# Performance work log

Measured on AMD Instinct MI355X. Metric: run time of the kernel, lower is better.

Reference implementation:

```python
import jax, jax.numpy as jnp
import numpy as np
from jax import lax

H = 8
C_HID = 32
LIDAR_DIM = 20
LIMITS = np.array([[1.0, 1.0, 3.1415927]], dtype=np.float32)


def _lidar_encoder(scans, w1, b1, w2, b2, wl, bl):
    # scans: [N, 20] -> Conv1d(1->16,k5,p2), ReLU, MaxPool(2), Conv1d(16->32,k3,p1), ReLU, global avg, Linear(32->5), ReLU
    x = scans[:, None, :]
    x = lax.conv_general_dilated(x, w1, (1,), [(2, 2)], dimension_numbers=('NCH', 'OIH', 'NCH')) + b1[None, :, None]
    x = jax.nn.relu(x)
    x = lax.reduce_window(x, -jnp.inf, lax.max, (1, 1, 2), (1, 1, 2), 'VALID')  # [N,16,10]
    x = lax.conv_general_dilated(x, w2, (1,), [(1, 1)], dimension_numbers=('NCH', 'OIH', 'NCH')) + b2[None, :, None]
    x = jax.nn.relu(x)
    x = jnp.mean(x, axis=2)  # AdaptiveAvgPool1d(1)+Flatten -> [N,32]
    return jax.nn.relu(x @ wl.T + bl)


def _gat_conv(x, src, dst, edge_attr, W, a_src, a_dst, We, a_e, bias, N):
    # PyG GATConv, heads=H, concat=True, edge_dim=1, leaky_relu slope 0.2, softmax over incoming edges (dst)
    xw = (x @ W).reshape(N, H, C_HID)
    als = jnp.sum(xw * a_src[None], -1)  # [N,H]
    ald = jnp.sum(xw * a_dst[None], -1)  # [N,H]
    ef = (edge_attr @ We).reshape(-1, H, C_HID)
    ale = jnp.sum(ef * a_e[None], -1)    # [E,H]
    alpha = jax.nn.leaky_relu(als[src] + ald[dst] + ale, 0.2)
    amax = jax.ops.segment_max(alpha, dst, num_segments=N)
    ex = jnp.exp(alpha - amax[dst])
    denom = jax.ops.segment_sum(ex, dst, num_segments=N)
    coef = ex / (denom[dst] + 1e-16)
    out = jax.ops.segment_sum(coef[:, :, None] * xw[src], dst, num_segments=N)
    return out.reshape(N, H * C_HID) + bias


def setup_inputs() -> dict:
    key = jax.random.key(0)
    ks = jax.random.split(key, 40)
    B, NPG, A = 1024, 16, 8
    N = B * NPG
    nodes = np.arange(NPG)
    s, d = np.meshgrid(nodes, nodes, indexing='ij')
    m = s != d
    s, d = s[m], d[m]  # fully-connected directed, no self loops (240 edges/graph)
    off = (np.arange(B) * NPG)[:, None]
    src = (off + s[None, :]).reshape(-1)
    dst = (off + d[None, :]).reshape(-1)
    E = src.shape[0]
    hid = C_HID
    def nrm(k, shape, sc=0.1):
        return jax.random.normal(k, shape, dtype=jnp.float32) * sc
    return {
        'x': jax.random.normal(ks[0], (N, 29), dtype=jnp.float32),
        'edge_index': jnp.asarray(np.stack([src, dst]).astype(np.int32)),
        'edge_attr': jax.random.uniform(ks[1], (E, 1), dtype=jnp.float32),
        'batch': jnp.asarray(np.repeat(np.arange(B), NPG).astype(np.int32)),
        'num_graphs': B,
        'num_agents': A,
        'lc_w1': nrm(ks[2], (16, 1, 5)), 'lc_b1': nrm(ks[3], (16,)),
        'lc_w2': nrm(ks[4], (32, 16, 3)), 'lc_b2': nrm(ks[5], (32,)),
        'lc_wl': nrm(ks[6], (5, 32)), 'lc_bl': nrm(ks[7], (5,)),
        'ld_w1': nrm(ks[8], (hid, 5)), 'ld_b1': nrm(ks[9], (hid,)),
        'ld_w2': nrm(ks[10], (LIDAR_DIM, hid)), 'ld_b2': nrm(ks[11], (LIDAR_DIM,)),
        'g1_W': nrm(ks[12], (6, H * hid)), 'g1_asrc': nrm(ks[13], (H, hid)), 'g1_adst': nrm(ks[14], (H, hid)), 'g1_We': nrm(ks[15], (1, H * hid)), 'g1_ae': nrm(ks[16], (H, hid)), 'g1_b': nrm(ks[17], (H * hid,)),
        'g2_W': nrm(ks[18], (H * hid, H * hid)), 'g2_asrc': nrm(ks[19], (H, hid)), 'g2_adst': nrm(ks[20], (H, hid)), 'g2_We': nrm(ks[21], (1, H * hid)), 'g2_ae': nrm(ks[22], (H, hid)), 'g2_b': nrm(ks[23], (H * hid,)),
        'g3_W': nrm(ks[24], (H * hid, H * hid)), 'g3_asrc': nrm(ks[25], (H, hid)), 'g3_adst': nrm(ks[26], (H, hid)), 'g3_We': nrm(ks[27], (1, H * hid)), 'g3_ae': nrm(ks[28], (H, hid)), 'g3_b': nrm(ks[29], (H * hid,)),
        'fc1_W': nrm(ks[30], (4 * hid, 16 * hid + 3)), 'fc1_b': nrm(ks[31], (4 * hid,)),
        'fc2_W': nrm(ks[32], (6, 4 * hid)), 'fc2_b': nrm(ks[33], (6,)),
    }


def reference(x, edge_index, edge_attr, batch, num_graphs, num_agents,
              lc_w1, lc_b1, lc_w2, lc_b2, lc_wl, lc_bl,
              ld_w1, ld_b1, ld_w2, ld_b2,
              g1_W, g1_asrc, g1_adst, g1_We, g1_ae, g1_b,
              g2_W, g2_asrc, g2_adst, g2_We, g2_ae, g2_b,
              g3_W, g3_asrc, g3_adst, g3_We, g3_ae, g3_b,
              fc1_W, fc1_b, fc2_W, fc2_b):
    N = x.shape[0]
    scans = x[:, :LIDAR_DIM]
    orig = x[:, LIDAR_DIM:LIDAR_DIM + 6]
    last_act = x[:, LIDAR_DIM + 6:]
    z = _lidar_encoder(scans, lc_w1, lc_b1, lc_w2, lc_b2, lc_wl, lc_bl)
    recon = jax.nn.relu(z @ ld_w1.T + ld_b1) @ ld_w2.T + ld_b2
    src, dst = edge_index[0], edge_index[1]
    # conv1: add_self_loops=False
    h = jax.nn.relu(_gat_conv(orig, src, dst, edge_attr, g1_W, g1_asrc, g1_adst, g1_We, g1_ae, g1_b, N))
    # conv2/conv3: add_self_loops=True with fill_value='mean' for edge_attr
    loop = jnp.arange(N, dtype=src.dtype)
    src2 = jnp.concatenate([src, loop])
    dst2 = jnp.concatenate([dst, loop])
    ea2 = jnp.concatenate([edge_attr, jnp.broadcast_to(jnp.mean(edge_attr, axis=0, keepdims=True), (N, 1))], axis=0)
    h = jax.nn.relu(_gat_conv(h, src2, dst2, ea2, g2_W, g2_asrc, g2_adst, g2_We, g2_ae, g2_b, N))
    h = jax.nn.relu(_gat_conv(h, src2, dst2, ea2, g3_W, g3_asrc, g3_adst, g3_We, g3_ae, g3_b, N))
    counts = jax.ops.segment_sum(jnp.ones((N,), jnp.float32), batch, num_segments=num_graphs)
    gemb = jax.ops.segment_sum(h, batch, num_segments=num_graphs) / counts[:, None]
    starts = jnp.searchsorted(batch, jnp.arange(num_graphs, dtype=batch.dtype))
    idx = (starts[:, None] + jnp.arange(num_agents)).reshape(-1)
    aemb = h[idx]
    la = last_act[idx]
    grep = jnp.repeat(gemb, num_agents, axis=0)
    comb = jnp.concatenate([aemb, grep, la], axis=1)
    hidn = jax.nn.relu(comb @ fc1_W.T + fc1_b)
    p = hidn @ fc2_W.T + fc2_b
    mean = jnp.tanh(p[:, :3]) * jnp.asarray(LIMITS)
    std = 0.01 + jax.nn.sigmoid(p[:, 3:]) * (0.3 - 0.01) + 1e-05
    return (mean.reshape(num_graphs, num_agents, -1), std.reshape(num_graphs, num_agents, -1), scans, recon)
```

## Files before the change

### kernel.cpp

```cpp
#include <hip/hip_runtime.h>
#include <math.h>

#define NODES   16384
#define NGRAPH  1024
#define EDGES   245760
#define EPG     240
#define FDIM    256

#define OUT_MEAN  0
#define OUT_STD   24576
#define OUT_SCANS 49152
#define OUT_RECON 376832

typedef __attribute__((ext_vector_type(4))) short bf16x4;
typedef __attribute__((ext_vector_type(8))) short bf16x8;
typedef __attribute__((ext_vector_type(4))) float f32x4;

static __device__ __forceinline__ float lrelu02(float v){ return v > 0.f ? v : 0.2f*v; }

static __device__ __forceinline__ unsigned short f2bf(float f){
    unsigned u = __float_as_uint(f);
    u = (u + 0x7FFFu + ((u >> 16) & 1u)) >> 16;
    return (unsigned short)u;
}
static __device__ __forceinline__ float bf2f(unsigned short h){
    return __uint_as_float(((unsigned)h) << 16);
}

__global__ __launch_bounds__(256) void prep_kernel(
    const float* __restrict__ x,  const float* __restrict__ ea,
    const float* __restrict__ W2, const float* __restrict__ as2, const float* __restrict__ ad2,
    const float* __restrict__ W3, const float* __restrict__ as3, const float* __restrict__ ad3,
    const float* __restrict__ W1, const float* __restrict__ as1, const float* __restrict__ ad1,
    const float* __restrict__ F1,
    const float* __restrict__ w1, const float* __restrict__ b1,
    const float* __restrict__ w2, const float* __restrict__ b2,
    const float* __restrict__ wl, const float* __restrict__ bl,
    const float* __restrict__ dw1, const float* __restrict__ db1,
    const float* __restrict__ dw2, const float* __restrict__ db2,
    unsigned short* __restrict__ T2, unsigned short* __restrict__ T3,
    unsigned short* __restrict__ T1, float* __restrict__ W1E,
    float* __restrict__ partial, float* __restrict__ out)
{
    __shared__ float red[256];
    __shared__ float sc[8][25];
    __shared__ float pooled[8][160];
    __shared__ float hid_lds[8][32];

    const int b = blockIdx.x;
    const int tid = threadIdx.x;

    if (b < 68) {
        const float* W   = (b < 34) ? W2 : W3;
        const float* as_ = (b < 34) ? as2 : as3;
        const float* ad_ = (b < 34) ? ad2 : ad3;
        unsigned short* T = (b < 34) ? T2 : T3;
        const int slot = ((b < 34) ? b : b - 34) * 256 + tid;
        const int nt = slot >> 9;
        const int rem = slot & 511;
        const int kk = rem >> 6;
        const int lane = rem & 63;
        const int ar = lane & 15, kgg = lane >> 4;
        const int col = nt * 16 + ar;
        unsigned short vals[8];
#pragma unroll
        for (int j = 0; j < 8; ++j) {
            const int k = kk * 32 + kgg * 4 + (j & 3) + ((j >> 2) << 4);
            float v;
            if (col < 256) v = W[k * 256 + col];
            else {
                const int j2 = col - 256, h = j2 & 7;
                const float* av = (j2 < 8) ? as_ : ad_;
                float s = 0.f;
                for (int c = 0; c < 32; ++c) s += W[k * 256 + h * 32 + c] * av[h * 32 + c];
                v = s;
            }
            vals[j] = f2bf(v);
        }
        *(bf16x8*)(T + (size_t)slot * 8) = *(const bf16x8*)vals;
        return;
    }
    if (b < 100) {
        const int slot = (b - 68) * 256 + tid;
        const int nt = slot >> 10;
        const int rem = slot & 1023;
        const int kk = rem >> 6;
        const int lane = rem & 63;
        const int o = nt * 16 + (lane & 15);
        const int kgg = lane >> 4;
        unsigned short vals[8];
#pragma unroll
        for (int j = 0; j < 8; ++j) {
            const int k = kk * 32 + kgg * 4 + (j & 3) + ((j >> 2) << 4);
            vals[j] = f2bf(F1[o * 515 + k]);
        }
        *(bf16x8*)(T1 + (size_t)slot * 8) = *(const bf16x8*)vals;
        return;
    }
    if (b == 100) {
        for (int c = tid; c < 272; c += 256) {
            for (int k = 0; k < 6; ++k) {
                float v;
                if (c < 256) v = W1[k * 256 + c];
                else {
                    const int j = c - 256, h = j & 7;
                    const float* av = (j < 8) ? as1 : ad1;
                    float s = 0.f;
                    for (int cc = 0; cc < 32; ++cc) s += W1[k * 256 + h * 32 + cc] * av[h * 32 + cc];
                    v = s;
                }
                W1E[k * 272 + c] = v;
            }
        }
        return;
    }
    if (b < 357) {
        const int base = (b - 101) * 960;
        float s = 0.f;
        for (int i = tid; i < 960; i += 256) s += ea[base + i];
        red[tid] = s; __syncthreads();
        for (int off = 128; off > 0; off >>= 1) {
            if (tid < off) red[tid] += red[tid + off];
            __syncthreads();
        }
        if (tid == 0) partial[b - 101] = red[0];
        return;
    }

    const int lane = tid & 31;
    const int nl   = tid >> 5;
    const int n    = (b - 357) * 8 + nl;

    if (lane < 20) {
        const float v = x[n * 29 + lane];
        sc[nl][lane + 2] = v;
        out[OUT_SCANS + n * 20 + lane] = v;
    } else if (lane < 25) {
        const int pads[5] = {0, 1, 22, 23, 24};
        sc[nl][pads[lane - 20]] = 0.f;
    }
    __syncthreads();

    {
        const int ic = lane & 15;
        const int hi = lane >> 4;
        float w1r[5];
#pragma unroll
        for (int k = 0; k < 5; ++k) w1r[k] = w1[ic * 5 + k];
        const float b1r = b1[ic];
#pragma unroll
        for (int q = 0; q < 5; ++q) {
            const int u  = 2 * q + hi;
            const int p0 = 2 * u;
            float a = b1r, bb = b1r;
#pragma unroll
            for (int k = 0; k < 5; ++k) {
                a  += sc[nl][p0 + k] * w1r[k];
                bb += sc[nl][p0 + 1 + k] * w1r[k];
            }
            pooled[nl][u * 16 + ic] = fmaxf(fmaxf(a, bb), 0.f);
        }
    }
    __syncthreads();

    float macc = 0.f;
    {
        float wreg[48];
#pragma unroll
        for (int i = 0; i < 12; ++i) {
            const float4 v4 = *(const float4*)&w2[lane * 48 + i * 4];
            wreg[i * 4 + 0] = v4.x; wreg[i * 4 + 1] = v4.y;
            wreg[i * 4 + 2] = v4.z; wreg[i * 4 + 3] = v4.w;
        }
        const float b2r = b2[lane];
        float pc[3][16];
#pragma unroll
        for (int i = 0; i < 4; ++i) {
            const float4 v0 = *(const float4*)&pooled[nl][0 * 16 + i * 4];
            const float4 v1 = *(const float4*)&pooled[nl][1 * 16 + i * 4];
            pc[0][i * 4 + 0] = v0.x; pc[0][i * 4 + 1] = v0.y; pc[0][i * 4 + 2] = v0.z; pc[0][i * 4 + 3] = v0.w;
            pc[1][i * 4 + 0] = v1.x; pc[1][i * 4 + 1] = v1.y; pc[1][i * 4 + 2] = v1.z; pc[1][i * 4 + 3] = v1.w;
            pc[2][i * 4 + 0] = 0.f;  pc[2][i * 4 + 1] = 0.f;  pc[2][i * 4 + 2] = 0.f;  pc[2][i * 4 + 3] = 0.f;
        }
#pragma unroll
        for (int t = 0; t < 10; ++t) {
            const int prev = (t + 2) % 3, cur = t % 3, nxt = (t + 1) % 3;
            if (t >= 1) {
                if (t + 1 <= 9) {
#pragma unroll
                    for (int i = 0; i < 4; ++i) {
                        const float4 v4 = *(const float4*)&pooled[nl][(t + 1) * 16 + i * 4];
                        pc[nxt][i * 4 + 0] = v4.x; pc[nxt][i * 4 + 1] = v4.y;
                        pc[nxt][i * 4 + 2] = v4.z; pc[nxt][i * 4 + 3] = v4.w;
                    }
                } else {
#pragma unroll
                    for (int ic = 0; ic < 16; ++ic) pc[nxt][ic] = 0.f;
                }
            }
            float v = b2r;
#pragma unroll
            for (int ic = 0; ic < 16; ++ic) {
                v += pc[prev][ic] * wreg[ic * 3 + 0]
                   + pc[cur][ic]  * wreg[ic * 3 + 1]
                   + pc[nxt][ic]  * wreg[ic * 3 + 2];
            }
            macc += fmaxf(v, 0.f);
        }
    }

    const float feat = macc * 0.1f;
    float z[5];
#pragma unroll
    for (int j = 0; j < 5; ++j) {
        float p = feat * wl[j * 32 + lane];
        p += __shfl_xor(p, 1);
        p += __shfl_xor(p, 2);
        p += __shfl_xor(p, 4);
        p += __shfl_xor(p, 8);
        p += __shfl_xor(p, 16);
        z[j] = fmaxf(bl[j] + p, 0.f);
    }
    float hv = db1[lane];
#pragma unroll
    for (int j = 0; j < 5; ++j) hv += z[j] * dw1[lane * 5 + j];
    hid_lds[nl][lane] = fmaxf(hv, 0.f);
    __syncthreads();

    if (lane < 20) {
        float acc = db2[lane];
#pragma unroll
        for (int k = 0; k < 32; ++k) acc += hid_lds[nl][k] * dw2[lane * 32 + k];
        out[OUT_RECON + n * 20 + lane] = acc;
    }
}

__global__ __launch_bounds__(512) void graph_kernel(
    const float* __restrict__ x,   const float* __restrict__ ea,
    const float* __restrict__ partial,
    const float* __restrict__ W1E,
    const float* __restrict__ g1_We, const float* __restrict__ g1_ae,
    const float* __restrict__ g1_b,
    const unsigned short* __restrict__ WTEf2,
    const float* __restrict__ g2_We, const float* __restrict__ g2_ae,
    const float* __restrict__ g2_b,
    const unsigned short* __restrict__ WTEf3,
    const float* __restrict__ g3_We, const float* __restrict__ g3_ae,
    const float* __restrict__ g3_b,
    const unsigned short* __restrict__ FT1f,
    const float* __restrict__ fc1W, const float* __restrict__ fc1b,
    const float* __restrict__ fc2W, const float* __restrict__ fc2b,
    float* __restrict__ out)
{
    __shared__ char hsb[2][8192] __attribute__((aligned(16)));
    __shared__ float salsald[2][16][16];
    __shared__ unsigned short coefb[2][8][16][20] __attribute__((aligned(8)));
    __shared__ float sS[8];
    __shared__ float hs6[2][16][6];
    __shared__ float lash[2][8][3];
    __shared__ float hidn[16][132];
    __shared__ unsigned short gembb[2][256] __attribute__((aligned(8)));
    __shared__ float ealds[480];

    const int tid = threadIdx.x;
    const int g0 = blockIdx.x * 2;
    const int lane = tid & 63, w = tid >> 6;
    const int arow = lane & 15, kg = lane >> 4;

    float eamean;
    {
        float pv = partial[lane] + partial[lane + 64] + partial[lane + 128] + partial[lane + 192];
        pv += __shfl_xor(pv, 1);
        pv += __shfl_xor(pv, 2);
        pv += __shfl_xor(pv, 4);
        pv += __shfl_xor(pv, 8);
        pv += __shfl_xor(pv, 16);
        pv += __shfl_xor(pv, 32);
        eamean = pv * (1.f / (float)EDGES);
    }

    if (tid < 192) {
        const int gg = tid / 96, t = tid % 96;
        hs6[gg][t / 6][t % 6] = x[((g0 + gg) * 16 + t / 6) * 29 + 20 + t % 6];
    } else if (tid < 240) {
        const int t = tid - 192, gg = t / 24, r = t % 24;
        lash[gg][r / 3][r % 3] = x[((g0 + gg) * 16 + r / 3) * 29 + 26 + r % 3];
    } else if (tid >= 248 && tid < 256) {
        const int h = tid - 248;
        float s = 0.f;
        for (int c = 0; c < 32; ++c) s += g1_We[h * 32 + c] * g1_ae[h * 32 + c];
        sS[h] = s;
    } else if (tid >= 256) {
        const int t = tid - 256;
        ealds[t] = ea[g0 * EPG + t];
        if (t < 224) ealds[t + 256] = ea[g0 * EPG + t + 256];
    }
    __syncthreads();

    float colA[16];
    {
        const int gg = tid >> 8, ht = tid & 255;
#pragma unroll
        for (int i = 0; i < 16; ++i) colA[i] = 0.f;
#pragma unroll
        for (int k = 0; k < 6; ++k) {
            const float wa = W1E[k * 272 + ht];
#pragma unroll
            for (int i = 0; i < 16; ++i) colA[i] += hs6[gg][i][k] * wa;
        }
        if (ht < 16) {
            float colC[16];
#pragma unroll
            for (int i = 0; i < 16; ++i) colC[i] = 0.f;
#pragma unroll
            for (int k = 0; k < 6; ++k) {
                const float wc = W1E[k * 272 + 256 + ht];
#pragma unroll
                for (int i = 0; i < 16; ++i) colC[i] += hs6[gg][i][k] * wc;
            }
#pragma unroll
            for (int i = 0; i < 16; ++i) salsald[gg][i][ht] = colC[i];
        }
    }
    __syncthreads();

    if (tid < 256) {
        const int gg = tid >> 7, row = tid & 127;
        const int d = row >> 3, h = row & 7;
        const float S = sS[h];
        const float aldv = salsald[gg][d][8 + h];
        float alf[16];
        float m = -1e30f;
#pragma unroll
        for (int s = 0; s < 16; ++s) {
            float a;
            if (s == d) a = -1e30f;
            else {
                const int el = s * 15 + d - (d > s ? 1 : 0);
                a = lrelu02(salsald[gg][s][h] + aldv + ealds[gg * EPG + el] * S);
            }
            alf[s] = a;
            m = fmaxf(m, a);
        }
        float sum = 0.f;
#pragma unroll
        for (int s = 0; s < 16; ++s) { alf[s] = expf(alf[s] - m); sum += alf[s]; }
        const float r = 1.f / (sum + 1e-16f);
#pragma unroll
        for (int s = 0; s < 16; ++s) coefb[gg][h][d][s] = f2bf(alf[s] * r);
    }
    __syncthreads();

    {
        const int gg = tid >> 8, c = tid & 255;
        const int h = c >> 5;
        const float b = g1_b[c];
#pragma unroll
        for (int d = 0; d < 16; ++d) {
            float v = b;
#pragma unroll
            for (int s4 = 0; s4 < 4; ++s4) {
                const bf16x4 cv = *(const bf16x4*)((const char*)&coefb[gg][0][0][0] + h * 640 + d * 40 + s4 * 8);
                v += bf2f((unsigned short)cv[0]) * colA[s4 * 4 + 0]
                   + bf2f((unsigned short)cv[1]) * colA[s4 * 4 + 1]
                   + bf2f((unsigned short)cv[2]) * colA[s4 * 4 + 2]
                   + bf2f((unsigned short)cv[3]) * colA[s4 * 4 + 3];
            }
            *(unsigned short*)(hsb[gg] + ((d * 512 + c * 2) ^ ((d & 7) << 4))) = f2bf(fmaxf(v, 0.f));
        }
    }
    __syncthreads();

#pragma unroll 1
    for (int ly = 0; ly < 2; ++ly) {
        const unsigned short* WT = ly ? WTEf3 : WTEf2;
        const float* We_ = ly ? g3_We : g2_We;
        const float* ae_ = ly ? g3_ae : g2_ae;
        const float* bi_ = ly ? g3_b  : g2_b;

        if (tid < 8) {
            float s = 0.f;
            for (int c = 0; c < 32; ++c) s += We_[tid * 32 + c] * ae_[tid * 32 + c];
            sS[tid] = s;
        }

        f32x4 acc[3][2];
#pragma unroll
        for (int t = 0; t < 3; ++t) { acc[t][0] = (f32x4){0,0,0,0}; acc[t][1] = (f32x4){0,0,0,0}; }
        {
            const int aswz = (arow & 7) << 4;
            for (int kk = 0; kk < 8; ++kk) {
                bf16x8 afr[2];
#pragma unroll
                for (int gg = 0; gg < 2; ++gg) {
                    const int ab = arow * 512 + kk * 64 + kg * 8;
                    const bf16x4 alo = *(const bf16x4*)(hsb[gg] + (ab ^ aswz));
                    const bf16x4 ahi = *(const bf16x4*)(hsb[gg] + ((ab + 32) ^ aswz));
                    afr[gg] = (bf16x8){alo[0], alo[1], alo[2], alo[3],
                                       ahi[0], ahi[1], ahi[2], ahi[3]};
                }
#pragma unroll
                for (int t = 0; t < 2; ++t) {
                    const int nt = t * 8 + w;
                    const bf16x8 bfr = *(const bf16x8*)(WT + (size_t)((nt * 8 + kk) * 64 + lane) * 8);
                    acc[t][0] = __builtin_amdgcn_mfma_f32_16x16x32_bf16(afr[0], bfr, acc[t][0], 0, 0, 0);
                    acc[t][1] = __builtin_amdgcn_mfma_f32_16x16x32_bf16(afr[1], bfr, acc[t][1], 0, 0, 0);
                }
                if (w == 0) {
                    const bf16x8 bfr = *(const bf16x8*)(WT + (size_t)((16 * 8 + kk) * 64 + lane) * 8);
                    acc[2][0] = __builtin_amdgcn_mfma_f32_16x16x32_bf16(afr[0], bfr, acc[2][0], 0, 0, 0);
                    acc[2][1] = __builtin_amdgcn_mfma_f32_16x16x32_bf16(afr[1], bfr, acc[2][1], 0, 0, 0);
                }
            }
        }
        if (w == 0) {
#pragma unroll
            for (int gg = 0; gg < 2; ++gg)
#pragma unroll
                for (int r = 0; r < 4; ++r) salsald[gg][kg * 4 + r][arow] = acc[2][gg][r];
        }
        __syncthreads();

        if (tid < 256) {
            const int gg = tid >> 7, row = tid & 127;
            const int d = row >> 3, h = row & 7;
            const float S = sS[h];
            const float aldv = salsald[gg][d][8 + h];
            float alf[16];
            float m = -1e30f;
#pragma unroll
            for (int s = 0; s < 16; ++s) {
                float a;
                if (s == d) a = lrelu02(salsald[gg][s][h] + aldv + eamean * S);
                else {
                    const int el = s * 15 + d - (d > s ? 1 : 0);
                    a = lrelu02(salsald[gg][s][h] + aldv + ealds[gg * EPG + el] * S);
                }
                alf[s] = a;
                m = fmaxf(m, a);
            }
            float sum = 0.f;
#pragma unroll
            for (int s = 0; s < 16; ++s) { alf[s] = expf(alf[s] - m); sum += alf[s]; }
            const float r = 1.f / (sum + 1e-16f);
#pragma unroll
            for (int s = 0; s < 16; ++s) coefb[gg][h][d][s] = f2bf(alf[s] * r);
        }
        __syncthreads();

        {
#pragma unroll
            for (int t = 0; t < 2; ++t) {
                const int nt = t * 8 + w;
                const int h = nt >> 1;
                const int c2 = nt * 16 + arow;
#pragma unroll
                for (int gg = 0; gg < 2; ++gg) {
                    const bf16x4 alo = *(const bf16x4*)((const char*)&coefb[gg][0][0][0] + h * 640 + arow * 40 + kg * 8);
                    const bf16x8 afrag = (bf16x8){alo[0], alo[1], alo[2], alo[3], 0, 0, 0, 0};
                    const bf16x8 bfr = (bf16x8){
                        (short)f2bf(acc[t][gg][0]), (short)f2bf(acc[t][gg][1]),
                        (short)f2bf(acc[t][gg][2]), (short)f2bf(acc[t][gg][3]),
                        0, 0, 0, 0};
                    f32x4 hacc = __builtin_amdgcn_mfma_f32_16x16x32_bf16(
                                     afrag, bfr, (f32x4){0.f, 0.f, 0.f, 0.f}, 0, 0, 0);
                    const float b = bi_[c2];
                    float p = 0.f;
#pragma unroll
                    for (int r = 0; r < 4; ++r) {
                        const float hv = fmaxf(hacc[r] + b, 0.f);
                        p += hv;
                        const int d = kg * 4 + r;
                        *(unsigned short*)(hsb[gg] + ((d * 512 + c2 * 2) ^ ((d & 7) << 4))) = f2bf(hv);
                    }
                    if (ly == 1) {
                        p += __shfl_xor(p, 16);
                        p += __shfl_xor(p, 32);
                        if (kg == 0) gembb[gg][c2] = f2bf(p * (1.f / 16.f));
                    }
                }
            }
        }
        __syncthreads();
    }

    {
        f32x4 acc2 = (f32x4){0,0,0,0};
        const int agg = arow >> 3, alr = arow & 7;
        const int aswz = (alr & 7) << 4;
        for (int kk = 0; kk < 16; ++kk) {
            bf16x4 alo, ahi;
            if (kk < 8) {
                const int ab = alr * 512 + kk * 64 + kg * 8;
                alo = *(const bf16x4*)(hsb[agg] + (ab ^ aswz));
                ahi = *(const bf16x4*)(hsb[agg] + ((ab + 32) ^ aswz));
            } else {
                const char* gp = (const char*)&gembb[agg][0] + (kk - 8) * 64 + kg * 8;
                alo = *(const bf16x4*)(gp);
                ahi = *(const bf16x4*)(gp + 32);
            }
            const bf16x8 afrag = (bf16x8){alo[0], alo[1], alo[2], alo[3],
                                          ahi[0], ahi[1], ahi[2], ahi[3]};
            const bf16x8 bfr = *(const bf16x8*)(FT1f + (size_t)((w * 16 + kk) * 64 + lane) * 8);
            acc2 = __builtin_amdgcn_mfma_f32_16x16x32_bf16(afrag, bfr, acc2, 0, 0, 0);
        }
        {
            const int o = w * 16 + arow;
            const float wl0 = fc1W[o * 515 + 512];
            const float wl1 = fc1W[o * 515 + 513];
            const float wl2 = fc1W[o * 515 + 514];
            const float b   = fc1b[o];
#pragma unroll
            for (int r = 0; r < 4; ++r) {
                const int row = kg * 4 + r;
                const int gg = row >> 3, ag = row & 7;
                float v = acc2[r] + b
                        + lash[gg][ag][0] * wl0 + lash[gg][ag][1] * wl1 + lash[gg][ag][2] * wl2;
                hidn[row][o] = fmaxf(v, 0.f);
            }
        }
    }
    __syncthreads();

    if (tid < 96) {
        const int a = tid / 6, j = tid % 6;
        const float* wr = &fc2W[j * 128];
        float acc = fc2b[j];
#pragma unroll
        for (int k = 0; k < 128; ++k) acc += wr[k] * hidn[a][k];
        const int gg = a >> 3, ag = a & 7;
        const int base = ((g0 + gg) * 8 + ag) * 3;
        if (j < 3) {
            const float lim = (j == 2) ? 3.1415927f : 1.0f;
            out[OUT_MEAN + base + j] = tanhf(acc) * lim;
        } else {
            const float sg = 1.f / (1.f + expf(-acc));
            out[OUT_STD + base + (j - 3)] = 0.01f + sg * (0.3f - 0.01f) + 1e-5f;
        }
    }
}

extern "C" void kernel_launch(void* const* d_in, const int* in_sizes, int n_in,
                              void* d_out, int out_size, void* d_ws, size_t ws_size,
                              hipStream_t stream)
{
    const float* x     = (const float*)d_in[0];
    const float* ea    = (const float*)d_in[2];
    const float* lc_w1 = (const float*)d_in[6];
    const float* lc_b1 = (const float*)d_in[7];
    const float* lc_w2 = (const float*)d_in[8];
    const float* lc_b2 = (const float*)d_in[9];
    const float* lc_wl = (const float*)d_in[10];
    const float* lc_bl = (const float*)d_in[11];
    const float* ld_w1 = (const float*)d_in[12];
    const float* ld_b1 = (const float*)d_in[13];
    const float* ld_w2 = (const float*)d_in[14];
    const float* ld_b2 = (const float*)d_in[15];
    const float* g1_W  = (const float*)d_in[16];
    const float* g1_as = (const float*)d_in[17];
    const float* g1_ad = (const float*)d_in[18];
    const float* g1_We = (const float*)d_in[19];
    const float* g1_ae = (const float*)d_in[20];
    const float* g1_b  = (const float*)d_in[21];
    const float* g2_W  = (const float*)d_in[22];
    const float* g2_as = (const float*)d_in[23];
    const float* g2_ad = (const float*)d_in[24];
    const float* g2_We = (const float*)d_in[25];
    const float* g2_ae = (const float*)d_in[26];
    const float* g2_b  = (const float*)d_in[27];
    const float* g3_W  = (const float*)d_in[28];
    const float* g3_as = (const float*)d_in[29];
    const float* g3_ad = (const float*)d_in[30];
    const float* g3_We = (const float*)d_in[31];
    const float* g3_ae = (const float*)d_in[32];
    const float* g3_b  = (const float*)d_in[33];
    const float* fc1_W = (const float*)d_in[34];
    const float* fc1_b = (const float*)d_in[35];
    const float* fc2_W = (const float*)d_in[36];
    const float* fc2_b = (const float*)d_in[37];

    float* out = (float*)d_out;
    unsigned short* WTEf2 = (unsigned short*)d_ws;
    unsigned short* WTEf3 = WTEf2 + 8704 * 8;
    unsigned short* FT1f  = WTEf3 + 8704 * 8;
    float* W1E    = (float*)(FT1f + 8192 * 8);
    float* partial = W1E + 6 * 272;

    prep_kernel<<<2405, 256, 0, stream>>>(x, ea,
                                          g2_W, g2_as, g2_ad,
                                          g3_W, g3_as, g3_ad,
                                          g1_W, g1_as, g1_ad,
                                          fc1_W,
                                          lc_w1, lc_b1, lc_w2, lc_b2, lc_wl, lc_bl,
                                          ld_w1, ld_b1, ld_w2, ld_b2,
                                          WTEf2, WTEf3, FT1f, W1E, partial, out);

    graph_kernel<<<512, 512, 0, stream>>>(x, ea, partial,
                                          W1E, g1_We, g1_ae, g1_b,
                                          WTEf2, g2_We, g2_ae, g2_b,
                                          WTEf3, g3_We, g3_ae, g3_b,
                                          FT1f, fc1_W, fc1_b, fc2_W, fc2_b, out);
}
```

Baseline: 73.51 us.

## Move lidar encoder/decoder blocks from prep kernel into graph kernel

The per-node lidar conv encoder and reconstruction decoder move out of the prep kernel and into extra blocks (index >= 512) of the graph kernel. These blocks process 16 nodes each and reuse the graph kernel's shared buffer. The prep kernel shrinks to the weight-packing and edge-attribute reduction blocks, so the critical path before the graph kernel gets shorter and the lidar work can overlap with the graph blocks. The cost is that the graph kernel's grid grows to 1536 blocks of 512 threads, with the larger LDS and register footprint of the graph path possibly limiting occupancy for the lidar blocks.

```diff
diff --git a/kernel.cpp b/kernel.cpp
--- a/kernel.cpp
+++ b/kernel.cpp
@@ -28,25 +28,16 @@
 }
 
 __global__ __launch_bounds__(256) void prep_kernel(
-    const float* __restrict__ x,  const float* __restrict__ ea,
+    const float* __restrict__ ea,
     const float* __restrict__ W2, const float* __restrict__ as2, const float* __restrict__ ad2,
     const float* __restrict__ W3, const float* __restrict__ as3, const float* __restrict__ ad3,
     const float* __restrict__ W1, const float* __restrict__ as1, const float* __restrict__ ad1,
     const float* __restrict__ F1,
-    const float* __restrict__ w1, const float* __restrict__ b1,
-    const float* __restrict__ w2, const float* __restrict__ b2,
-    const float* __restrict__ wl, const float* __restrict__ bl,
-    const float* __restrict__ dw1, const float* __restrict__ db1,
-    const float* __restrict__ dw2, const float* __restrict__ db2,
     unsigned short* __restrict__ T2, unsigned short* __restrict__ T3,
     unsigned short* __restrict__ T1, float* __restrict__ W1E,
-    float* __restrict__ partial, float* __restrict__ out)
+    float* __restrict__ partial)
 {
     __shared__ float red[256];
-    __shared__ float sc[8][25];
-    __shared__ float pooled[8][160];
-    __shared__ float hid_lds[8][32];
-
     const int b = blockIdx.x;
     const int tid = threadIdx.x;
 
@@ -114,7 +105,7 @@
         }
         return;
     }
-    if (b < 357) {
+    {
         const int base = (b - 101) * 960;
         float s = 0.f;
         for (int i = tid; i < 960; i += 256) s += ea[base + i];
@@ -124,114 +115,6 @@
             __syncthreads();
         }
         if (tid == 0) partial[b - 101] = red[0];
-        return;
-    }
-
-    const int lane = tid & 31;
-    const int nl   = tid >> 5;
-    const int n    = (b - 357) * 8 + nl;
-
-    if (lane < 20) {
-        const float v = x[n * 29 + lane];
-        sc[nl][lane + 2] = v;
-        out[OUT_SCANS + n * 20 + lane] = v;
-    } else if (lane < 25) {
-        const int pads[5] = {0, 1, 22, 23, 24};
-        sc[nl][pads[lane - 20]] = 0.f;
-    }
-    __syncthreads();
-
-    {
-        const int ic = lane & 15;
-        const int hi = lane >> 4;
-        float w1r[5];
-#pragma unroll
-        for (int k = 0; k < 5; ++k) w1r[k] = w1[ic * 5 + k];
-        const float b1r = b1[ic];
-#pragma unroll
-        for (int q = 0; q < 5; ++q) {
-            const int u  = 2 * q + hi;
-            const int p0 = 2 * u;
-            float a = b1r, bb = b1r;
-#pragma unroll
-            for (int k = 0; k < 5; ++k) {
-                a  += sc[nl][p0 + k] * w1r[k];
-                bb += sc[nl][p0 + 1 + k] * w1r[k];
-            }
-            pooled[nl][u * 16 + ic] = fmaxf(fmaxf(a, bb), 0.f);
-        }
-    }
-    __syncthreads();
-
-    float macc = 0.f;
-    {
-        float wreg[48];
-#pragma unroll
-        for (int i = 0; i < 12; ++i) {
-            const float4 v4 = *(const float4*)&w2[lane * 48 + i * 4];
-            wreg[i * 4 + 0] = v4.x; wreg[i * 4 + 1] = v4.y;
-            wreg[i * 4 + 2] = v4.z; wreg[i * 4 + 3] = v4.w;
-        }
-        const float b2r = b2[lane];
-        float pc[3][16];
-#pragma unroll
-        for (int i = 0; i < 4; ++i) {
-            const float4 v0 = *(const float4*)&pooled[nl][0 * 16 + i * 4];
-            const float4 v1 = *(const float4*)&pooled[nl][1 * 16 + i * 4];
-            pc[0][i * 4 + 0] = v0.x; pc[0][i * 4 + 1] = v0.y; pc[0][i * 4 + 2] = v0.z; pc[0][i * 4 + 3] = v0.w;
-            pc[1][i * 4 + 0] = v1.x; pc[1][i * 4 + 1] = v1.y; pc[1][i * 4 + 2] = v1.z; pc[1][i * 4 + 3] = v1.w;
-            pc[2][i * 4 + 0] = 0.f;  pc[2][i * 4 + 1] = 0.f;  pc[2][i * 4 + 2] = 0.f;  pc[2][i * 4 + 3] = 0.f;
-        }
-#pragma unroll
-        for (int t = 0; t < 10; ++t) {
-            const int prev = (t + 2) % 3, cur = t % 3, nxt = (t + 1) % 3;
-            if (t >= 1) {
-                if (t + 1 <= 9) {
-#pragma unroll
-                    for (int i = 0; i < 4; ++i) {
-                        const float4 v4 = *(const float4*)&pooled[nl][(t + 1) * 16 + i * 4];
-                        pc[nxt][i * 4 + 0] = v4.x; pc[nxt][i * 4 + 1] = v4.y;
-                        pc[nxt][i * 4 + 2] = v4.z; pc[nxt][i * 4 + 3] = v4.w;
-                    }
-                } else {
-#pragma unroll
-                    for (int ic = 0; ic < 16; ++ic) pc[nxt][ic] = 0.f;
-                }
-            }
-            float v = b2r;
-#pragma unroll
-            for (int ic = 0; ic < 16; ++ic) {
-                v += pc[prev][ic] * wreg[ic * 3 + 0]
-                   + pc[cur][ic]  * wreg[ic * 3 + 1]
-                   + pc[nxt][ic]  * wreg[ic * 3 + 2];
-            }
-            macc += fmaxf(v, 0.f);
-        }
-    }
-
-    const float feat = macc * 0.1f;
-    float z[5];
-#pragma unroll
-    for (int j = 0; j < 5; ++j) {
-        float p = feat * wl[j * 32 + lane];
-        p += __shfl_xor(p, 1);
-        p += __shfl_xor(p, 2);
-        p += __shfl_xor(p, 4);
-        p += __shfl_xor(p, 8);
-        p += __shfl_xor(p, 16);
-        z[j] = fmaxf(bl[j] + p, 0.f);
-    }
-    float hv = db1[lane];
-#pragma unroll
-    for (int j = 0; j < 5; ++j) hv += z[j] * dw1[lane * 5 + j];
-    hid_lds[nl][lane] = fmaxf(hv, 0.f);
-    __syncthreads();
-
-    if (lane < 20) {
-        float acc = db2[lane];
-#pragma unroll
-        for (int k = 0; k < 32; ++k) acc += hid_lds[nl][k] * dw2[lane * 32 + k];
-        out[OUT_RECON + n * 20 + lane] = acc;
     }
 }
 
@@ -250,6 +133,11 @@
     const unsigned short* __restrict__ FT1f,
     const float* __restrict__ fc1W, const float* __restrict__ fc1b,
     const float* __restrict__ fc2W, const float* __restrict__ fc2b,
+    const float* __restrict__ w1, const float* __restrict__ b1,
+    const float* __restrict__ w2, const float* __restrict__ b2,
+    const float* __restrict__ wl, const float* __restrict__ bl,
+    const float* __restrict__ dw1, const float* __restrict__ db1,
+    const float* __restrict__ dw2, const float* __restrict__ db2,
     float* __restrict__ out)
 {
     __shared__ char hsb[2][8192] __attribute__((aligned(16)));
@@ -263,6 +151,121 @@
     __shared__ float ealds[480];
 
     const int tid = threadIdx.x;
+
+    if (blockIdx.x >= 512) {
+        float* scb = (float*)&hsb[0][0];
+        float* plb = scb + 16 * 25;
+        float* hdb = plb + 16 * 160;
+
+        const int lane = tid & 31;
+        const int nl   = tid >> 5;
+        const int n    = (blockIdx.x - 512) * 16 + nl;
+
+        if (lane < 20) {
+            const float v = x[n * 29 + lane];
+            scb[nl * 25 + lane + 2] = v;
+            out[OUT_SCANS + n * 20 + lane] = v;
+        } else if (lane < 25) {
+            const int pads[5] = {0, 1, 22, 23, 24};
+            scb[nl * 25 + pads[lane - 20]] = 0.f;
+        }
+        __syncthreads();
+
+        {
+            const int ic = lane & 15;
+            const int hi = lane >> 4;
+            float w1r[5];
+#pragma unroll
+            for (int k = 0; k < 5; ++k) w1r[k] = w1[ic * 5 + k];
+            const float b1r = b1[ic];
+#pragma unroll
+            for (int q = 0; q < 5; ++q) {
+                const int u  = 2 * q + hi;
+                const int p0 = 2 * u;
+                float a = b1r, bb = b1r;
+#pragma unroll
+                for (int k = 0; k < 5; ++k) {
+                    a  += scb[nl * 25 + p0 + k] * w1r[k];
+                    bb += scb[nl * 25 + p0 + 1 + k] * w1r[k];
+                }
+                plb[nl * 160 + u * 16 + ic] = fmaxf(fmaxf(a, bb), 0.f);
+            }
+        }
+        __syncthreads();
+
+        float macc = 0.f;
+        {
+            float wreg[48];
+#pragma unroll
+            for (int i = 0; i < 12; ++i) {
+                const float4 v4 = *(const float4*)&w2[lane * 48 + i * 4];
+                wreg[i * 4 + 0] = v4.x; wreg[i * 4 + 1] = v4.y;
+                wreg[i * 4 + 2] = v4.z; wreg[i * 4 + 3] = v4.w;
+            }
+            const float b2r = b2[lane];
+            float pc[3][16];
+#pragma unroll
+            for (int i = 0; i < 4; ++i) {
+                const float4 v0 = *(const float4*)&plb[nl * 160 + 0 * 16 + i * 4];
+                const float4 v1 = *(const float4*)&plb[nl * 160 + 1 * 16 + i * 4];
+                pc[0][i * 4 + 0] = v0.x; pc[0][i * 4 + 1] = v0.y; pc[0][i * 4 + 2] = v0.z; pc[0][i * 4 + 3] = v0.w;
+                pc[1][i * 4 + 0] = v1.x; pc[1][i * 4 + 1] = v1.y; pc[1][i * 4 + 2] = v1.z; pc[1][i * 4 + 3] = v1.w;
+                pc[2][i * 4 + 0] = 0.f;  pc[2][i * 4 + 1] = 0.f;  pc[2][i * 4 + 2] = 0.f;  pc[2][i * 4 + 3] = 0.f;
+            }
+#pragma unroll
+            for (int t = 0; t < 10; ++t) {
+                const int prev = (t + 2) % 3, cur = t % 3, nxt = (t + 1) % 3;
+                if (t >= 1) {
+                    if (t + 1 <= 9) {
+#pragma unroll
+                        for (int i = 0; i < 4; ++i) {
+                            const float4 v4 = *(const float4*)&plb[nl * 160 + (t + 1) * 16 + i * 4];
+                            pc[nxt][i * 4 + 0] = v4.x; pc[nxt][i * 4 + 1] = v4.y;
+                            pc[nxt][i * 4 + 2] = v4.z; pc[nxt][i * 4 + 3] = v4.w;
+                        }
+                    } else {
+#pragma unroll
+                        for (int ic = 0; ic < 16; ++ic) pc[nxt][ic] = 0.f;
+                    }
+                }
+                float v = b2r;
+#pragma unroll
+                for (int ic = 0; ic < 16; ++ic) {
+                    v += pc[prev][ic] * wreg[ic * 3 + 0]
+                       + pc[cur][ic]  * wreg[ic * 3 + 1]
+                       + pc[nxt][ic]  * wreg[ic * 3 + 2];
+                }
+                macc += fmaxf(v, 0.f);
+            }
+        }
+
+        const float feat = macc * 0.1f;
+        float z[5];
+#pragma unroll
+        for (int j = 0; j < 5; ++j) {
+            float p = feat * wl[j * 32 + lane];
+            p += __shfl_xor(p, 1);
+            p += __shfl_xor(p, 2);
+            p += __shfl_xor(p, 4);
+            p += __shfl_xor(p, 8);
+            p += __shfl_xor(p, 16);
+            z[j] = fmaxf(bl[j] + p, 0.f);
+        }
+        float hv = db1[lane];
+#pragma unroll
+        for (int j = 0; j < 5; ++j) hv += z[j] * dw1[lane * 5 + j];
+        hdb[nl * 32 + lane] = fmaxf(hv, 0.f);
+        __syncthreads();
+
+        if (lane < 20) {
+            float acc = db2[lane];
+#pragma unroll
+            for (int k = 0; k < 32; ++k) acc += hdb[nl * 32 + k] * dw2[lane * 32 + k];
+            out[OUT_RECON + n * 20 + lane] = acc;
+        }
+        return;
+    }
+
     const int g0 = blockIdx.x * 2;
     const int lane = tid & 63, w = tid >> 6;
     const int arow = lane & 15, kg = lane >> 4;
@@ -586,18 +589,19 @@
     float* W1E    = (float*)(FT1f + 8192 * 8);
     float* partial = W1E + 6 * 272;
 
-    prep_kernel<<<2405, 256, 0, stream>>>(x, ea,
-                                          g2_W, g2_as, g2_ad,
-                                          g3_W, g3_as, g3_ad,
-                                          g1_W, g1_as, g1_ad,
-                                          fc1_W,
-                                          lc_w1, lc_b1, lc_w2, lc_b2, lc_wl, lc_bl,
-                                          ld_w1, ld_b1, ld_w2, ld_b2,
-                                          WTEf2, WTEf3, FT1f, W1E, partial, out);
-
-    graph_kernel<<<512, 512, 0, stream>>>(x, ea, partial,
-                                          W1E, g1_We, g1_ae, g1_b,
-                                          WTEf2, g2_We, g2_ae, g2_b,
-                                          WTEf3, g3_We, g3_ae, g3_b,
-                                          FT1f, fc1_W, fc1_b, fc2_W, fc2_b, out);
+    prep_kernel<<<357, 256, 0, stream>>>(ea,
+                                         g2_W, g2_as, g2_ad,
+                                         g3_W, g3_as, g3_ad,
+                                         g1_W, g1_as, g1_ad,
+                                         fc1_W,
+                                         WTEf2, WTEf3, FT1f, W1E, partial);
+
+    graph_kernel<<<1536, 512, 0, stream>>>(x, ea, partial,
+                                           W1E, g1_We, g1_ae, g1_b,
+                                           WTEf2, g2_We, g2_ae, g2_b,
+                                           WTEf3, g3_We, g3_ae, g3_b,
+                                           FT1f, fc1_W, fc1_b, fc2_W, fc2_b,
+                                           lc_w1, lc_b1, lc_w2, lc_b2, lc_wl, lc_bl,
+                                           ld_w1, ld_b1, ld_w2, ld_b2,
+                                           out);
 }
```

Measured after the change: 88.65 us. 1.21x slower.

## Process one graph per block instead of two in graph kernel

Applied to the files above, without the earlier changes.

The graph kernel now handles a single graph per 512-thread block and launches 1024 blocks instead of 512, halving per-block shared memory and state. Each weight fragment loaded for the MFMA layers is now reused across one graph instead of two, and many threads sit idle in the scalar phases. The intent is more blocks and better occupancy, at the cost of twice the weight-fragment traffic and half-empty MFMA tiles in the final FC layer.

```diff
diff --git a/kernel.cpp b/kernel.cpp
--- a/kernel.cpp
+++ b/kernel.cpp
@@ -252,18 +252,18 @@
     const float* __restrict__ fc2W, const float* __restrict__ fc2b,
     float* __restrict__ out)
 {
-    __shared__ char hsb[2][8192] __attribute__((aligned(16)));
-    __shared__ float salsald[2][16][16];
-    __shared__ unsigned short coefb[2][8][16][20] __attribute__((aligned(8)));
+    __shared__ char hsb[8192] __attribute__((aligned(16)));
+    __shared__ float salsald[16][16];
+    __shared__ unsigned short coefb[8][16][20] __attribute__((aligned(8)));
     __shared__ float sS[8];
-    __shared__ float hs6[2][16][6];
-    __shared__ float lash[2][8][3];
-    __shared__ float hidn[16][132];
-    __shared__ unsigned short gembb[2][256] __attribute__((aligned(8)));
-    __shared__ float ealds[480];
+    __shared__ float hs6[16][6];
+    __shared__ float lash[8][3];
+    __shared__ float hidn[8][132];
+    __shared__ unsigned short gembb[256] __attribute__((aligned(8)));
+    __shared__ float ealds[240];
 
     const int tid = threadIdx.x;
-    const int g0 = blockIdx.x * 2;
+    const int g = blockIdx.x;
     const int lane = tid & 63, w = tid >> 6;
     const int arow = lane & 15, kg = lane >> 4;
 
@@ -279,56 +279,42 @@
         eamean = pv * (1.f / (float)EDGES);
     }
 
-    if (tid < 192) {
-        const int gg = tid / 96, t = tid % 96;
-        hs6[gg][t / 6][t % 6] = x[((g0 + gg) * 16 + t / 6) * 29 + 20 + t % 6];
-    } else if (tid < 240) {
-        const int t = tid - 192, gg = t / 24, r = t % 24;
-        lash[gg][r / 3][r % 3] = x[((g0 + gg) * 16 + r / 3) * 29 + 26 + r % 3];
+    if (tid < 96) {
+        hs6[tid / 6][tid % 6] = x[(g * 16 + tid / 6) * 29 + 20 + tid % 6];
+    } else if (tid < 120) {
+        const int t = tid - 96;
+        lash[t / 3][t % 3] = x[(g * 16 + t / 3) * 29 + 26 + t % 3];
     } else if (tid >= 248 && tid < 256) {
         const int h = tid - 248;
         float s = 0.f;
         for (int c = 0; c < 32; ++c) s += g1_We[h * 32 + c] * g1_ae[h * 32 + c];
         sS[h] = s;
-    } else if (tid >= 256) {
-        const int t = tid - 256;
-        ealds[t] = ea[g0 * EPG + t];
-        if (t < 224) ealds[t + 256] = ea[g0 * EPG + t + 256];
+    } else if (tid >= 256 && tid < 496) {
+        ealds[tid - 256] = ea[g * EPG + (tid - 256)];
     }
     __syncthreads();
 
     float colA[16];
-    {
-        const int gg = tid >> 8, ht = tid & 255;
+    if (tid < 272) {
 #pragma unroll
         for (int i = 0; i < 16; ++i) colA[i] = 0.f;
 #pragma unroll
         for (int k = 0; k < 6; ++k) {
-            const float wa = W1E[k * 272 + ht];
-#pragma unroll
-            for (int i = 0; i < 16; ++i) colA[i] += hs6[gg][i][k] * wa;
-        }
-        if (ht < 16) {
-            float colC[16];
-#pragma unroll
-            for (int i = 0; i < 16; ++i) colC[i] = 0.f;
-#pragma unroll
-            for (int k = 0; k < 6; ++k) {
-                const float wc = W1E[k * 272 + 256 + ht];
-#pragma unroll
-                for (int i = 0; i < 16; ++i) colC[i] += hs6[gg][i][k] * wc;
-            }
-#pragma unroll
-            for (int i = 0; i < 16; ++i) salsald[gg][i][ht] = colC[i];
-        }
-    }
-    __syncthreads();
-
-    if (tid < 256) {
-        const int gg = tid >> 7, row = tid & 127;
-        const int d = row >> 3, h = row & 7;
+            const float wa = W1E[k * 272 + tid];
+#pragma unroll
+            for (int i = 0; i < 16; ++i) colA[i] += hs6[i][k] * wa;
+        }
+        if (tid >= 256) {
+#pragma unroll
+            for (int i = 0; i < 16; ++i) salsald[i][tid - 256] = colA[i];
+        }
+    }
+    __syncthreads();
+
+    if (tid < 128) {
+        const int d = tid >> 3, h = tid & 7;
         const float S = sS[h];
-        const float aldv = salsald[gg][d][8 + h];
+        const float aldv = salsald[d][8 + h];
         float alf[16];
         float m = -1e30f;
 #pragma unroll
@@ -337,7 +323,7 @@
             if (s == d) a = -1e30f;
             else {
                 const int el = s * 15 + d - (d > s ? 1 : 0);
-                a = lrelu02(salsald[gg][s][h] + aldv + ealds[gg * EPG + el] * S);
+                a = lrelu02(salsald[s][h] + aldv + ealds[el] * S);
             }
             alf[s] = a;
             m = fmaxf(m, a);
@@ -347,12 +333,12 @@
         for (int s = 0; s < 16; ++s) { alf[s] = expf(alf[s] - m); sum += alf[s]; }
         const float r = 1.f / (sum + 1e-16f);
 #pragma unroll
-        for (int s = 0; s < 16; ++s) coefb[gg][h][d][s] = f2bf(alf[s] * r);
-    }
-    __syncthreads();
-
-    {
-        const int gg = tid >> 8, c = tid & 255;
+        for (int s = 0; s < 16; ++s) coefb[h][d][s] = f2bf(alf[s] * r);
+    }
+    __syncthreads();
+
+    if (tid < 256) {
+        const int c = tid;
         const int h = c >> 5;
         const float b = g1_b[c];
 #pragma unroll
@@ -360,13 +346,13 @@
             float v = b;
 #pragma unroll
             for (int s4 = 0; s4 < 4; ++s4) {
-                const bf16x4 cv = *(const bf16x4*)((const char*)&coefb[gg][0][0][0] + h * 640 + d * 40 + s4 * 8);
+                const bf16x4 cv = *(const bf16x4*)((const char*)&coefb[0][0][0] + h * 640 + d * 40 + s4 * 8);
                 v += bf2f((unsigned short)cv[0]) * colA[s4 * 4 + 0]
                    + bf2f((unsigned short)cv[1]) * colA[s4 * 4 + 1]
                    + bf2f((unsigned short)cv[2]) * colA[s4 * 4 + 2]
                    + bf2f((unsigned short)cv[3]) * colA[s4 * 4 + 3];
             }
-            *(unsigned short*)(hsb[gg] + ((d * 512 + c * 2) ^ ((d & 7) << 4))) = f2bf(fmaxf(v, 0.f));
+            *(unsigned short*)(hsb + ((d * 512 + c * 2) ^ ((d & 7) << 4))) = f2bf(fmaxf(v, 0.f));
         }
     }
     __syncthreads();
@@ -384,57 +370,48 @@
             sS[tid] = s;
         }
 
-        f32x4 acc[3][2];
-#pragma unroll
-        for (int t = 0; t < 3; ++t) { acc[t][0] = (f32x4){0,0,0,0}; acc[t][1] = (f32x4){0,0,0,0}; }
+        f32x4 acc[3];
+#pragma unroll
+        for (int t = 0; t < 3; ++t) acc[t] = (f32x4){0,0,0,0};
         {
             const int aswz = (arow & 7) << 4;
             for (int kk = 0; kk < 8; ++kk) {
-                bf16x8 afr[2];
-#pragma unroll
-                for (int gg = 0; gg < 2; ++gg) {
-                    const int ab = arow * 512 + kk * 64 + kg * 8;
-                    const bf16x4 alo = *(const bf16x4*)(hsb[gg] + (ab ^ aswz));
-                    const bf16x4 ahi = *(const bf16x4*)(hsb[gg] + ((ab + 32) ^ aswz));
-                    afr[gg] = (bf16x8){alo[0], alo[1], alo[2], alo[3],
-                                       ahi[0], ahi[1], ahi[2], ahi[3]};
-                }
+                const int ab = arow * 512 + kk * 64 + kg * 8;
+                const bf16x4 alo = *(const bf16x4*)(hsb + (ab ^ aswz));
+                const bf16x4 ahi = *(const bf16x4*)(hsb + ((ab + 32) ^ aswz));
+                const bf16x8 afr = (bf16x8){alo[0], alo[1], alo[2], alo[3],
+                                            ahi[0], ahi[1], ahi[2], ahi[3]};
 #pragma unroll
                 for (int t = 0; t < 2; ++t) {
                     const int nt = t * 8 + w;
                     const bf16x8 bfr = *(const bf16x8*)(WT + (size_t)((nt * 8 + kk) * 64 + lane) * 8);
-                    acc[t][0] = __builtin_amdgcn_mfma_f32_16x16x32_bf16(afr[0], bfr, acc[t][0], 0, 0, 0);
-                    acc[t][1] = __builtin_amdgcn_mfma_f32_16x16x32_bf16(afr[1], bfr, acc[t][1], 0, 0, 0);
+                    acc[t] = __builtin_amdgcn_mfma_f32_16x16x32_bf16(afr, bfr, acc[t], 0, 0, 0);
                 }
                 if (w == 0) {
                     const bf16x8 bfr = *(const bf16x8*)(WT + (size_t)((16 * 8 + kk) * 64 + lane) * 8);
-                    acc[2][0] = __builtin_amdgcn_mfma_f32_16x16x32_bf16(afr[0], bfr, acc[2][0], 0, 0, 0);
-                    acc[2][1] = __builtin_amdgcn_mfma_f32_16x16x32_bf16(afr[1], bfr, acc[2][1], 0, 0, 0);
+                    acc[2] = __builtin_amdgcn_mfma_f32_16x16x32_bf16(afr, bfr, acc[2], 0, 0, 0);
                 }
             }
         }
         if (w == 0) {
 #pragma unroll
-            for (int gg = 0; gg < 2; ++gg)
-#pragma unroll
-                for (int r = 0; r < 4; ++r) salsald[gg][kg * 4 + r][arow] = acc[2][gg][r];
+            for (int r = 0; r < 4; ++r) salsald[kg * 4 + r][arow] = acc[2][r];
         }
         __syncthreads();
 
-        if (tid < 256) {
-            const int gg = tid >> 7, row = tid & 127;
-            const int d = row >> 3, h = row & 7;
+        if (tid < 128) {
+            const int d = tid >> 3, h = tid & 7;
             const float S = sS[h];
-            const float aldv = salsald[gg][d][8 + h];
+            const float aldv = salsald[d][8 + h];
             float alf[16];
             float m = -1e30f;
 #pragma unroll
             for (int s = 0; s < 16; ++s) {
                 float a;
-                if (s == d) a = lrelu02(salsald[gg][s][h] + aldv + eamean * S);
+                if (s == d) a = lrelu02(salsald[s][h] + aldv + eamean * S);
                 else {
                     const int el = s * 15 + d - (d > s ? 1 : 0);
-                    a = lrelu02(salsald[gg][s][h] + aldv + ealds[gg * EPG + el] * S);
+                    a = lrelu02(salsald[s][h] + aldv + ealds[el] * S);
                 }
                 alf[s] = a;
                 m = fmaxf(m, a);
@@ -444,7 +421,7 @@
             for (int s = 0; s < 16; ++s) { alf[s] = expf(alf[s] - m); sum += alf[s]; }
             const float r = 1.f / (sum + 1e-16f);
 #pragma unroll
-            for (int s = 0; s < 16; ++s) coefb[gg][h][d][s] = f2bf(alf[s] * r);
+            for (int s = 0; s < 16; ++s) coefb[h][d][s] = f2bf(alf[s] * r);
         }
         __syncthreads();
 
@@ -454,30 +431,27 @@
                 const int nt = t * 8 + w;
                 const int h = nt >> 1;
                 const int c2 = nt * 16 + arow;
-#pragma unroll
-                for (int gg = 0; gg < 2; ++gg) {
-                    const bf16x4 alo = *(const bf16x4*)((const char*)&coefb[gg][0][0][0] + h * 640 + arow * 40 + kg * 8);
-                    const bf16x8 afrag = (bf16x8){alo[0], alo[1], alo[2], alo[3], 0, 0, 0, 0};
-                    const bf16x8 bfr = (bf16x8){
-                        (short)f2bf(acc[t][gg][0]), (short)f2bf(acc[t][gg][1]),
-                        (short)f2bf(acc[t][gg][2]), (short)f2bf(acc[t][gg][3]),
-                        0, 0, 0, 0};
-                    f32x4 hacc = __builtin_amdgcn_mfma_f32_16x16x32_bf16(
-                                     afrag, bfr, (f32x4){0.f, 0.f, 0.f, 0.f}, 0, 0, 0);
-                    const float b = bi_[c2];
-                    float p = 0.f;
-#pragma unroll
-                    for (int r = 0; r < 4; ++r) {
-                        const float hv = fmaxf(hacc[r] + b, 0.f);
-                        p += hv;
-                        const int d = kg * 4 + r;
-                        *(unsigned short*)(hsb[gg] + ((d * 512 + c2 * 2) ^ ((d & 7) << 4))) = f2bf(hv);
-                    }
-                    if (ly == 1) {
-                        p += __shfl_xor(p, 16);
-                        p += __shfl_xor(p, 32);
-                        if (kg == 0) gembb[gg][c2] = f2bf(p * (1.f / 16.f));
-                    }
+                const bf16x4 alo = *(const bf16x4*)((const char*)&coefb[0][0][0] + h * 640 + arow * 40 + kg * 8);
+                const bf16x8 afrag = (bf16x8){alo[0], alo[1], alo[2], alo[3], 0, 0, 0, 0};
+                const bf16x8 bfr = (bf16x8){
+                    (short)f2bf(acc[t][0]), (short)f2bf(acc[t][1]),
+                    (short)f2bf(acc[t][2]), (short)f2bf(acc[t][3]),
+                    0, 0, 0, 0};
+                f32x4 hacc = __builtin_amdgcn_mfma_f32_16x16x32_bf16(
+                                 afrag, bfr, (f32x4){0.f, 0.f, 0.f, 0.f}, 0, 0, 0);
+                const float b = bi_[c2];
+                float p = 0.f;
+#pragma unroll
+                for (int r = 0; r < 4; ++r) {
+                    const float hv = fmaxf(hacc[r] + b, 0.f);
+                    p += hv;
+                    const int d = kg * 4 + r;
+                    *(unsigned short*)(hsb + ((d * 512 + c2 * 2) ^ ((d & 7) << 4))) = f2bf(hv);
+                }
+                if (ly == 1) {
+                    p += __shfl_xor(p, 16);
+                    p += __shfl_xor(p, 32);
+                    if (kg == 0) gembb[c2] = f2bf(p * (1.f / 16.f));
                 }
             }
         }
@@ -486,16 +460,16 @@
 
     {
         f32x4 acc2 = (f32x4){0,0,0,0};
-        const int agg = arow >> 3, alr = arow & 7;
+        const int alr = arow & 7;
         const int aswz = (alr & 7) << 4;
         for (int kk = 0; kk < 16; ++kk) {
             bf16x4 alo, ahi;
             if (kk < 8) {
                 const int ab = alr * 512 + kk * 64 + kg * 8;
-                alo = *(const bf16x4*)(hsb[agg] + (ab ^ aswz));
-                ahi = *(const bf16x4*)(hsb[agg] + ((ab + 32) ^ aswz));
+                alo = *(const bf16x4*)(hsb + (ab ^ aswz));
+                ahi = *(const bf16x4*)(hsb + ((ab + 32) ^ aswz));
             } else {
-                const char* gp = (const char*)&gembb[agg][0] + (kk - 8) * 64 + kg * 8;
+                const char* gp = (const char*)&gembb[0] + (kk - 8) * 64 + kg * 8;
                 alo = *(const bf16x4*)(gp);
                 ahi = *(const bf16x4*)(gp + 32);
             }
@@ -513,23 +487,23 @@
 #pragma unroll
             for (int r = 0; r < 4; ++r) {
                 const int row = kg * 4 + r;
-                const int gg = row >> 3, ag = row & 7;
-                float v = acc2[r] + b
-                        + lash[gg][ag][0] * wl0 + lash[gg][ag][1] * wl1 + lash[gg][ag][2] * wl2;
-                hidn[row][o] = fmaxf(v, 0.f);
-            }
-        }
-    }
-    __syncthreads();
-
-    if (tid < 96) {
+                if (row < 8) {
+                    float v = acc2[r] + b
+                            + lash[row][0] * wl0 + lash[row][1] * wl1 + lash[row][2] * wl2;
+                    hidn[row][o] = fmaxf(v, 0.f);
+                }
+            }
+        }
+    }
+    __syncthreads();
+
+    if (tid < 48) {
         const int a = tid / 6, j = tid % 6;
         const float* wr = &fc2W[j * 128];
         float acc = fc2b[j];
 #pragma unroll
         for (int k = 0; k < 128; ++k) acc += wr[k] * hidn[a][k];
-        const int gg = a >> 3, ag = a & 7;
-        const int base = ((g0 + gg) * 8 + ag) * 3;
+        const int base = (g * 8 + a) * 3;
         if (j < 3) {
             const float lim = (j == 2) ? 3.1415927f : 1.0f;
             out[OUT_MEAN + base + j] = tanhf(acc) * lim;
@@ -595,9 +569,9 @@
                                           ld_w1, ld_b1, ld_w2, ld_b2,
                                           WTEf2, WTEf3, FT1f, W1E, partial, out);
 
-    graph_kernel<<<512, 512, 0, stream>>>(x, ea, partial,
-                                          W1E, g1_We, g1_ae, g1_b,
-                                          WTEf2, g2_We, g2_ae, g2_b,
-                                          WTEf3, g3_We, g3_ae, g3_b,
-                                          FT1f, fc1_W, fc1_b, fc2_W, fc2_b, out);
+    graph_kernel<<<1024, 512, 0, stream>>>(x, ea, partial,
+                                           W1E, g1_We, g1_ae, g1_b,
+                                           WTEf2, g2_We, g2_ae, g2_b,
+                                           WTEf3, g3_We, g3_ae, g3_b,
+                                           FT1f, fc1_W, fc1_b, fc2_W, fc2_b, out);
 }
```

Result: slower. 75.19 us (+2.3%).
